# Performance work log

Hardware: AMD Instinct MI355X
Metric: run time of the kernel (lower is better)

The kernel has to match this reference:

```python
import jax, jax.numpy as jnp
import numpy as np
from jax import lax

INPUT_SIZE = 16384
NUM_CONV = 128
KMAX = 11  # max kernel size from {7, 9, 11}
BATCH = 256


def setup_inputs() -> dict:
    # Mirror FeatureExtractor._generate_random_params / _generate_random_convolutions
    rng = np.random.RandomState(0)
    kernel_sizes = rng.choice([7, 9, 11], NUM_CONV)
    dilations, paddings = [], []
    W = np.zeros((NUM_CONV, KMAX), np.float32)  # zero-padded kernel bank
    b = np.zeros((NUM_CONV,), np.float32)
    for i, k in enumerate(kernel_sizes):
        d_f = 2.0 ** rng.uniform(0.0, np.log2((INPUT_SIZE - 1) / (k - 1)))
        p = (k - 1) * d_f // 2 if rng.randint(2) else 0
        dilations.append(int(d_f))
        paddings.append(int(p))
        w = rng.normal(0.0, 1.0, k)
        w = w - w.mean()  # centered kernel ('normal' sampling type)
        W[i, :k] = w.astype(np.float32)
        b[i] = rng.uniform(-1.0, 1.0)
    key = jax.random.key(0)
    x = jax.random.normal(key, (BATCH, 1, INPUT_SIZE), dtype=jnp.float32)
    return {
        "x": x,
        "weights": jnp.asarray(W),
        "biases": jnp.asarray(b),
        "kernel_sizes": np.asarray(kernel_sizes, np.int64),
        "dilations": np.asarray(dilations, np.int64),
        "paddings": np.asarray(paddings, np.int64),
    }


def reference(x, weights, biases, kernel_sizes, dilations, paddings):
    # x: [B, 1, L]. Each conv has its own (k, dilation, padding) -> distinct
    # output lengths, so a Python loop over the fixed NUM_CONV structurally
    # distinct convs is required (matches the original module).
    feats = []
    n = weights.shape[0]
    for i in range(n):
        k = int(kernel_sizes[i])
        d = int(dilations[i])
        p = int(paddings[i])
        w = weights[i, :k].reshape(1, 1, k)  # OIW
        # torch Conv1d = cross-correlation with rhs (kernel) dilation
        y = lax.conv_general_dilated(
            x, w, window_strides=(1,), padding=[(p, p)], rhs_dilation=(d,)
        ) + biases[i]
        fm = y[:, 0, :]                      # [B, L_out]
        mx = fm.max(axis=-1)                 # global max pool
        ppv = (fm >= 0).sum(axis=-1) / fm.shape[-1]  # proportion of positives
        feats.append(jnp.stack([mx, ppv.astype(x.dtype)], axis=-1))  # [B, 2]
    out = jnp.concatenate(feats, axis=-1)    # [B, 2*num_conv], interleaved (max, ppv)
    return out.reshape(out.shape[0], 1, out.shape[1])  # [B, 1, 2*num_conv]
```

## Files before the change

### kernel.cpp

```cpp
#include <hip/hip_runtime.h>
#include <math.h>

#define S_LEN   16384
#define NCONV   128
#define NBATCH  256
#define TPB     1024
#define NGRP    8
#define ZSLOT   16384
#define DSTRIDE 24
#define BIGQ    (1 << 28)

typedef float __attribute__((address_space(1))) as1_float;
typedef float __attribute__((address_space(3))) as3_float;
typedef __attribute__((ext_vector_type(2))) float f2;
typedef unsigned long long u64;

__global__ void setup_desc(const int* __restrict__ ks, const int* __restrict__ dil,
                           const int* __restrict__ pad, const float* __restrict__ W,
                           const float* __restrict__ bias, int* __restrict__ ws)
{
  __shared__ int cost_s[NCONV];
  __shared__ int grp_s[NCONV];
  const int ci = threadIdx.x;
  const int is64 = (ks[1] == 0);
  const int k = is64 ? ks[2 * ci]  : ks[ci];
  const int d = is64 ? dil[2 * ci] : dil[ci];
  const int p = is64 ? pad[2 * ci] : pad[ci];
  const int L = S_LEN + 2 * p - d * (k - 1);
  const int A = L / d, B = L - A * d;
  int cost = L * (k + 9) + d * k * 3;
  if (d == 1) cost += L * (k + 9);
  cost_s[ci] = cost;
  __syncthreads();
  int rank = 0;
  for (int j = 0; j < NCONV; ++j) {
    const int cj = cost_s[j];
    rank += (cj > cost) || (cj == cost && j < ci);
  }
  int gg = rank & 7;
  if ((rank >> 3) & 1) gg = 7 - gg;
  grp_s[ci] = gg;
  __syncthreads();
  int rho = 0;
  for (int j = 0; j < NCONV; ++j) {
    if (grp_s[j] != gg) continue;
    const int cj = cost_s[j];
    rho += (cj > cost) || (cj == cost && j < ci);
  }
#pragma unroll
  for (int h = 0; h < 2; ++h) {
    const int j2 = 2 * rho + h;
    const int wv = (j2 < 16) ? j2 : 31 - j2;
    const int sq = (j2 < 16) ? 0 : 1;
    int* dsc = ws + (gg * 32 + wv * 2 + sq) * DSTRIDE;
    dsc[0] = d; dsc[1] = p; dsc[2] = A; dsc[3] = B;
    dsc[4] = ci; dsc[5] = rho; dsc[6] = h; dsc[7] = k;
    ((float*)dsc)[8] = 1.0f / (float)L;
    ((float*)dsc)[9] = bias[ci];
#pragma unroll
    for (int t = 0; t < 11; ++t) ((float*)dsc)[10 + t] = W[ci * 11 + t];
  }
}

__device__ __forceinline__ float sgpr_f(float v) {
  return __int_as_float(__builtin_amdgcn_readfirstlane(__float_as_int(v)));
}
__device__ __forceinline__ int sgpr_i(int v) {
  return __builtin_amdgcn_readfirstlane(v);
}
__device__ __forceinline__ float rcpf(float x) { return __builtin_amdgcn_rcpf(x); }

__device__ __forceinline__ int divq(int num, float rd, int d) {
  int q = (int)((float)num * rd);
  q -= (q * d > num);
  q += ((q + 1) * d <= num);
  return q;
}

__device__ __forceinline__ float lds_at(const float* sh, int pos) {
  unsigned idx = (unsigned)pos;
  idx = idx > (unsigned)ZSLOT ? (unsigned)ZSLOT : idx;
  return sh[idx];
}
__device__ __forceinline__ f2 rd2(const float* sh, int pos) {
  unsigned idx = (unsigned)pos;
  idx = idx > (unsigned)ZSLOT ? (unsigned)ZSLOT : idx;
  f2 v; v.x = sh[idx]; v.y = sh[idx + 1];
  return v;
}

__device__ __forceinline__ f2 pfma(f2 a, f2 b, f2 c) {
#if __has_builtin(__builtin_elementwise_fma)
  return __builtin_elementwise_fma(a, b, c);
#else
  f2 r; r.x = fmaf(a.x, b.x, c.x); r.y = fmaf(a.y, b.y, c.y); return r;
#endif
}
__device__ __forceinline__ f2 pmax(f2 a, f2 b) {
#if __has_builtin(__builtin_elementwise_max)
  return __builtin_elementwise_max(a, b);
#else
  f2 r; r.x = fmaxf(a.x, b.x); r.y = fmaxf(a.y, b.y); return r;
#endif
}

template <int K>
__device__ __forceinline__ void pwalk(
    const float* sh, const u64* wu, float bval,
    int d, int sb, int q0, int q1, f2& mxv, int& ca, int& cb)
{
  const int n = q1 - q0;
  if (n <= 0) return;
  f2 win[K];
  int pos = sb + q0 * d;
#pragma unroll
  for (int t = 0; t < K - 1; ++t) { win[t] = rd2(sh, pos); pos += d; }
  f2 bb; bb.x = bval; bb.y = bval;
  int i = 0;
  for (; i + K <= n; i += K) {
#pragma unroll
    for (int s = 0; s < K; ++s) {
      const f2 cur = rd2(sh, pos); pos += d;
      f2 a = bb;
#pragma unroll
      for (int t = 0; t < K; ++t) {
        const f2 wv = __builtin_bit_cast(f2, wu[t]);
        a = pfma(wv, (t == K - 1) ? cur : win[(s + t) % K], a);
      }
      win[(s + K - 1) % K] = cur;
      mxv = pmax(mxv, a);
      ca += (a.x >= 0.f); cb += (a.y >= 0.f);
    }
  }
  const int rem = n - i;
  if (rem > 0) {
#pragma unroll
    for (int s = 0; s < K - 1; ++s) {
      const f2 cur = rd2(sh, pos); pos += d;
      f2 a = bb;
#pragma unroll
      for (int t = 0; t < K; ++t) {
        const f2 wv = __builtin_bit_cast(f2, wu[t]);
        a = pfma(wv, (t == K - 1) ? cur : win[(s + t) % K], a);
      }
      win[(s + K - 1) % K] = cur;
      if (s < rem) { mxv = pmax(mxv, a); ca += (a.x >= 0.f); cb += (a.y >= 0.f); }
    }
  }
}

__device__ __forceinline__ void swalk(
    const float* sh, const float* w, float bval,
    int d, int sb, int q0, int q1, float& mx, int& cnt)
{
  const int n = q1 - q0;
  if (n <= 0) return;
  float win[11];
  int pos = sb + q0 * d;
#pragma unroll
  for (int t = 0; t < 10; ++t) { win[t] = lds_at(sh, pos); pos += d; }
  int i = 0;
  for (; i + 11 <= n; i += 11) {
#pragma unroll
    for (int s = 0; s < 11; ++s) {
      win[(s + 10) % 11] = lds_at(sh, pos); pos += d;
      float a = bval;
#pragma unroll
      for (int t = 0; t < 11; ++t) a = fmaf(w[t], win[(s + t) % 11], a);
      mx = fmaxf(mx, a); cnt += (a >= 0.f);
    }
  }
  const int rem = n - i;
  if (rem > 0) {
#pragma unroll
    for (int s = 0; s < 10; ++s) {
      win[(s + 10) % 11] = lds_at(sh, pos); pos += d;
      float a = bval;
#pragma unroll
      for (int t = 0; t < 11; ++t) a = fmaf(w[t], win[(s + t) % 11], a);
      if (s < rem) { mx = fmaxf(mx, a); cnt += (a >= 0.f); }
    }
  }
}

__device__ __forceinline__ void scalar_split(
    const float* sh, const float* w, float bval,
    int d, int p, int r, int c0, int c1, int lane, float& mx, int& cnt)
{
  const int n = c1 - c0;
  if (n <= 0) return;
  const int v  = lane;
  const int mm = n >> 6;
  const int sA = (mm >= 32) ? (v & 31) : (((v & 31) * mm) >> 5);
  const int vB = v + 1;
  const int sB = (mm >= 32) ? (vB & 31) : (((vB & 31) * mm) >> 5);
  const int q0 = c0 + (int)(((long long)n * v) >> 6) + sA;
  const int q1 = (v == 63) ? c1 : c0 + (int)(((long long)n * vB) >> 6) + sB;
  swalk(sh, w, bval, d, r - p, q0, q1, mx, cnt);
}

template <int K>
__device__ __forceinline__ void one_out(
    const float* sh, const float* w, float bval,
    int d, int p, int j, float& mx, int& cnt)
{
  float a = bval;
  int pos = j - p;
#pragma unroll
  for (int t = 0; t < K; ++t) { a = fmaf(w[t], lds_at(sh, pos), a); pos += d; }
  mx = fmaxf(mx, a); cnt += (a >= 0.f);
}

template <int K>
__device__ __forceinline__ void conv_chunk(
    const float* sh, const u64* wu, const float* w, float bval,
    int d, int p, int A, int B, int h, int lane,
    f2& mxv, float& mxs, int& ca, int& cb)
{
  if (d == 1) {
    const int H = (A + 1) >> 1;
    scalar_split(sh, w, bval, 1, p, 0, h ? H : 0, h ? A : H, lane, mxs, ca);
    return;
  }
  const int npair = d >> 1;
  if (npair >= 128) {
    const int half = npair >> 1;
    const int g0 = h ? half : 0;
    const int g1 = h ? npair : half;
    for (int c = g0 + lane; c < g1; c += 64) {
      const int r0 = 2 * c;
      const int Qm = A + (r0 + 1 < B);
      pwalk<K>(sh, wu, bval, d, r0 - p, 0, Qm, mxv, ca, cb);
      if (B == r0 + 1) one_out<K>(sh, w, bval, d, p, r0 + A * d, mxs, ca);
    }
  } else if (npair >= 64) {
    const int H = (A + 1) >> 1;
    const int c0 = h ? H : 0;
    const int c1 = h ? BIGQ : H;
    for (int c = lane; c < npair; c += 64) {
      const int r0 = 2 * c;
      const int Qm = A + (r0 + 1 < B);
      pwalk<K>(sh, wu, bval, d, r0 - p, c0, min(c1, Qm), mxv, ca, cb);
      if (B == r0 + 1 && A >= c0 && A < c1)
        one_out<K>(sh, w, bval, d, p, r0 + A * d, mxs, ca);
    }
  } else {
    const int H = (A + 1) >> 1;
    const int c0 = h ? H : 0;
    const int c1h = h ? BIGQ : H;
    const float rdp = rcpf((float)npair);
    int v  = (int)((float)lane * rdp);
    int g2 = lane - v * npair;
    if (g2 < 0)           { --v; g2 += npair; }
    else if (g2 >= npair) { ++v; g2 -= npair; }
    const int nv = divq(63 - g2, rdp, npair) + 1;
    const int r0 = 2 * g2;
    const int Qm = A + (r0 + 1 < B);
    const int cc1 = min(c1h, Qm);
    const int n = cc1 - c0;
    if (n > 0) {
      const float rn = rcpf((float)nv);
      const int mm = (int)((float)n * rn);
      const int sA = (mm >= 32) ? (v & 31) : (((v & 31) * mm) >> 5);
      const int vB = v + 1;
      const int sB = (mm >= 32) ? (vB & 31) : (((vB & 31) * mm) >> 5);
      const int q0 = c0 + (int)((float)(n * v) * rn) + sA;
      const int q1 = (v == nv - 1) ? cc1
                   : c0 + (int)((float)(n * vB) * rn) + sB;
      pwalk<K>(sh, wu, bval, d, r0 - p, q0, q1, mxv, ca, cb);
    }
    if (v == nv - 1 && B == r0 + 1 && A >= c0 && A < c1h)
      one_out<K>(sh, w, bval, d, p, r0 + A * d, mxs, ca);
  }
  if ((d & 1) && d > 1) {
    const int H2 = (A + 1) >> 1;
    const int r = d - 1;
    const int Qr = A + (r < B);
    const int c0 = h ? H2 : 0;
    const int c1 = h ? Qr : min(H2, Qr);
    scalar_split(sh, w, bval, d, p, r, c0, c1, lane, mxs, ca);
  }
}

__global__ __launch_bounds__(TPB, 8) void rocket_feats(
    const float* __restrict__ x, const int* __restrict__ ws,
    float* __restrict__ out)
{
  __shared__ float sh[S_LEN + 2];
  __shared__ float smx[2][16];
  __shared__ int   scn[2][16];
  __shared__ int   sci[16];
  __shared__ float sin_[16];

  const int tid  = threadIdx.x;
  const int blk  = blockIdx.x;
  const int g    = blk & 7;
  const int b    = blk >> 3;
  const int lane = tid & 63, wid = tid >> 6;

  const float* xrow = x + (size_t)b * S_LEN;
  {
    const float* gb = xrow + lane * 4;
#pragma unroll
    for (int c = 0; c < 4; ++c) {
      const int off = (wid * 4 + c) * 256;
      __builtin_amdgcn_global_load_lds((const as1_float*)(gb + off),
                                       (as3_float*)(sh + off), 16, 0, 0);
    }
  }
  if (tid == 0) { sh[ZSLOT] = 0.f; sh[ZSLOT + 1] = 0.f; }
  __syncthreads();

  for (int sq = 0; sq < 2; ++sq) {
    const int* dsc = ws + (g * 32 + wid * 2 + sq) * DSTRIDE;
    const int d  = sgpr_i(dsc[0]);
    const int p  = sgpr_i(dsc[1]);
    const int A  = sgpr_i(dsc[2]);
    const int B  = sgpr_i(dsc[3]);
    const int ci = sgpr_i(dsc[4]);
    const int t_ = sgpr_i(dsc[5]);
    const int h  = sgpr_i(dsc[6]);
    const int k  = sgpr_i(dsc[7]);
    const float invL = sgpr_f(((const float*)dsc)[8]);
    const float bval = sgpr_f(((const float*)dsc)[9]);
    float wf[11]; u64 wu[11];
#pragma unroll
    for (int t = 0; t < 11; ++t) {
      wf[t] = sgpr_f(((const float*)dsc)[10 + t]);
      const unsigned wb = (unsigned)__float_as_int(wf[t]);
      wu[t] = ((u64)wb << 32) | (u64)wb;
    }

    f2 mxv; mxv.x = -INFINITY; mxv.y = -INFINITY;
    float mxs = -INFINITY;
    int ca = 0, cb = 0;

    if (k == 7)
      conv_chunk<7 >(sh, wu, wf, bval, d, p, A, B, h, lane, mxv, mxs, ca, cb);
    else if (k == 9)
      conv_chunk<9 >(sh, wu, wf, bval, d, p, A, B, h, lane, mxv, mxs, ca, cb);
    else
      conv_chunk<11>(sh, wu, wf, bval, d, p, A, B, h, lane, mxv, mxs, ca, cb);

    float mx = fmaxf(fmaxf(mxv.x, mxv.y), mxs);
    int cnt = ca + cb;
#pragma unroll
    for (int off = 32; off > 0; off >>= 1) {
      mx = fmaxf(mx, __shfl_down(mx, off, 64));
      cnt += __shfl_down(cnt, off, 64);
    }
    if (lane == 0) {
      smx[h][t_] = mx; scn[h][t_] = cnt;
      sci[t_] = ci; sin_[t_] = invL;
    }
  }

  __syncthreads();
  if (tid < 16) {
    const float m = fmaxf(smx[0][tid], smx[1][tid]);
    const int   c = scn[0][tid] + scn[1][tid];
    out[(size_t)b * (2 * NCONV) + 2 * sci[tid]]     = m;
    out[(size_t)b * (2 * NCONV) + 2 * sci[tid] + 1] = (float)c * sin_[tid];
  }
}

extern "C" void kernel_launch(void* const* d_in, const int* in_sizes, int n_in,
                              void* d_out, int out_size, void* d_ws, size_t ws_size,
                              hipStream_t stream) {
  const float* x    = (const float*)d_in[0];
  const float* W    = (const float*)d_in[1];
  const float* bias = (const float*)d_in[2];
  const int*   ks   = (const int*)d_in[3];
  const int*   dil  = (const int*)d_in[4];
  const int*   pad  = (const int*)d_in[5];
  float* out = (float*)d_out;
  int*   ws  = (int*)d_ws;

  hipLaunchKernelGGL(setup_desc, dim3(1), dim3(NCONV), 0, stream,
                     ks, dil, pad, W, bias, ws);
  hipLaunchKernelGGL(rocket_feats, dim3(NBATCH * NGRP), dim3(TPB), 0, stream,
                     x, ws, out);
}
```

Baseline: 297.6 us.

## Use wave-ballot counting, byte-offset LDS addressing, templated scalar walk and retuned cost model

Positive counts are now accumulated as wave-uniform scalar values using ballot plus popcount. This removes the per-lane integer adds and the shuffle reduction for counts, at the cost of a ballot per output. LDS addressing switches to precomputed byte offsets with a shifted buffer that has zero guard slots on both sides. This is meant to cut address arithmetic. The scalar walk is templated on kernel size so k=7/9 no longer do 11 taps, and the load-balancing cost model used for grouping convolutions is retuned.

```diff
diff --git a/kernel.cpp b/kernel.cpp
--- a/kernel.cpp
+++ b/kernel.cpp
@@ -6,9 +6,9 @@
 #define NBATCH  256
 #define TPB     1024
 #define NGRP    8
-#define ZSLOT   16384
 #define DSTRIDE 24
 #define BIGQ    (1 << 28)
+#define CLMP    65552u
 
 typedef float __attribute__((address_space(1))) as1_float;
 typedef float __attribute__((address_space(3))) as3_float;
@@ -28,8 +28,8 @@
   const int p = is64 ? pad[2 * ci] : pad[ci];
   const int L = S_LEN + 2 * p - d * (k - 1);
   const int A = L / d, B = L - A * d;
-  int cost = L * (k + 9) + d * k * 3;
-  if (d == 1) cost += L * (k + 9);
+  int cost = L * (k + 5) + ((d >= 128) ? (d >> 1) : 64) * (k - 1) * 2;
+  if (d == 1) cost = L * (k + 5) * 2;
   cost_s[ci] = cost;
   __syncthreads();
   int rank = 0;
@@ -77,16 +77,17 @@
   return q;
 }
 
-__device__ __forceinline__ float lds_at(const float* sh, int pos) {
-  unsigned idx = (unsigned)pos;
-  idx = idx > (unsigned)ZSLOT ? (unsigned)ZSLOT : idx;
-  return sh[idx];
-}
-__device__ __forceinline__ f2 rd2(const float* sh, int pos) {
-  unsigned idx = (unsigned)pos;
-  idx = idx > (unsigned)ZSLOT ? (unsigned)ZSLOT : idx;
-  f2 v; v.x = sh[idx]; v.y = sh[idx + 1];
+__device__ __forceinline__ f2 rd2b(const float* sh, int ib) {
+  unsigned u = (unsigned)ib;
+  u = u > CLMP ? CLMP : u;
+  const float* p = (const float*)((const char*)sh + u);
+  f2 v; v.x = p[0]; v.y = p[1];
   return v;
+}
+__device__ __forceinline__ float ld1b(const float* sh, int ib) {
+  unsigned u = (unsigned)ib;
+  u = u > CLMP ? CLMP : u;
+  return *(const float*)((const char*)sh + u);
 }
 
 __device__ __forceinline__ f2 pfma(f2 a, f2 b, f2 c) {
@@ -103,89 +104,108 @@
   f2 r; r.x = fmaxf(a.x, b.x); r.y = fmaxf(a.y, b.y); return r;
 #endif
 }
+__device__ __forceinline__ int wcount(bool pred) {
+  return (int)__popcll(__ballot(pred));
+}
 
 template <int K>
 __device__ __forceinline__ void pwalk(
-    const float* sh, const u64* wu, float bval,
-    int d, int sb, int q0, int q1, f2& mxv, int& ca, int& cb)
+    const float* sh, const u64* wu, const f2 bbv,
+    int d, int sb4, int q0, int q1, f2& mxv, int& cw)
 {
   const int n = q1 - q0;
   if (n <= 0) return;
   f2 win[K];
-  int pos = sb + q0 * d;
-#pragma unroll
-  for (int t = 0; t < K - 1; ++t) { win[t] = rd2(sh, pos); pos += d; }
-  f2 bb; bb.x = bval; bb.y = bval;
+  int bb = (sb4 + q0 * d) * 4;
+#pragma unroll
+  for (int t = 0; t < K - 1; ++t)
+    win[t] = rd2b(sh, bb + t * (d * 4));
+  bb += (K - 1) * (d * 4);
   int i = 0;
   for (; i + K <= n; i += K) {
 #pragma unroll
     for (int s = 0; s < K; ++s) {
-      const f2 cur = rd2(sh, pos); pos += d;
-      f2 a = bb;
-#pragma unroll
-      for (int t = 0; t < K; ++t) {
-        const f2 wv = __builtin_bit_cast(f2, wu[t]);
-        a = pfma(wv, (t == K - 1) ? cur : win[(s + t) % K], a);
-      }
+      const f2 cur = rd2b(sh, bb + s * (d * 4));
+      f2 a = pfma(__builtin_bit_cast(f2, wu[0]), win[s % K], bbv);
+#pragma unroll
+      for (int t = 1; t < K; ++t)
+        a = pfma(__builtin_bit_cast(f2, wu[t]),
+                 (t == K - 1) ? cur : win[(s + t) % K], a);
       win[(s + K - 1) % K] = cur;
       mxv = pmax(mxv, a);
-      ca += (a.x >= 0.f); cb += (a.y >= 0.f);
-    }
+      cw += wcount(a.x >= 0.f);
+      cw += wcount(a.y >= 0.f);
+    }
+    bb += K * (d * 4);
   }
   const int rem = n - i;
   if (rem > 0) {
 #pragma unroll
     for (int s = 0; s < K - 1; ++s) {
-      const f2 cur = rd2(sh, pos); pos += d;
-      f2 a = bb;
-#pragma unroll
-      for (int t = 0; t < K; ++t) {
-        const f2 wv = __builtin_bit_cast(f2, wu[t]);
-        a = pfma(wv, (t == K - 1) ? cur : win[(s + t) % K], a);
-      }
+      const f2 cur = rd2b(sh, bb + s * (d * 4));
+      f2 a = pfma(__builtin_bit_cast(f2, wu[0]), win[s % K], bbv);
+#pragma unroll
+      for (int t = 1; t < K; ++t)
+        a = pfma(__builtin_bit_cast(f2, wu[t]),
+                 (t == K - 1) ? cur : win[(s + t) % K], a);
       win[(s + K - 1) % K] = cur;
-      if (s < rem) { mxv = pmax(mxv, a); ca += (a.x >= 0.f); cb += (a.y >= 0.f); }
-    }
-  }
-}
-
+      const bool ok = (s < rem);
+      if (ok) mxv = pmax(mxv, a);
+      cw += wcount(ok && (a.x >= 0.f));
+      cw += wcount(ok && (a.y >= 0.f));
+    }
+  }
+}
+
+template <int K>
 __device__ __forceinline__ void swalk(
     const float* sh, const float* w, float bval,
-    int d, int sb, int q0, int q1, float& mx, int& cnt)
+    int d, int sb4, int q0, int q1, float& mx, int& cw)
 {
   const int n = q1 - q0;
   if (n <= 0) return;
-  float win[11];
-  int pos = sb + q0 * d;
-#pragma unroll
-  for (int t = 0; t < 10; ++t) { win[t] = lds_at(sh, pos); pos += d; }
+  float win[K];
+  int bb = (sb4 + q0 * d) * 4;
+#pragma unroll
+  for (int t = 0; t < K - 1; ++t)
+    win[t] = ld1b(sh, bb + t * (d * 4));
+  bb += (K - 1) * (d * 4);
   int i = 0;
-  for (; i + 11 <= n; i += 11) {
-#pragma unroll
-    for (int s = 0; s < 11; ++s) {
-      win[(s + 10) % 11] = lds_at(sh, pos); pos += d;
-      float a = bval;
-#pragma unroll
-      for (int t = 0; t < 11; ++t) a = fmaf(w[t], win[(s + t) % 11], a);
-      mx = fmaxf(mx, a); cnt += (a >= 0.f);
-    }
+  for (; i + K <= n; i += K) {
+#pragma unroll
+    for (int s = 0; s < K; ++s) {
+      const float cur = ld1b(sh, bb + s * (d * 4));
+      float a = fmaf(w[0], win[s % K], bval);
+#pragma unroll
+      for (int t = 1; t < K; ++t)
+        a = fmaf(w[t], (t == K - 1) ? cur : win[(s + t) % K], a);
+      win[(s + K - 1) % K] = cur;
+      mx = fmaxf(mx, a);
+      cw += wcount(a >= 0.f);
+    }
+    bb += K * (d * 4);
   }
   const int rem = n - i;
   if (rem > 0) {
 #pragma unroll
-    for (int s = 0; s < 10; ++s) {
-      win[(s + 10) % 11] = lds_at(sh, pos); pos += d;
-      float a = bval;
-#pragma unroll
-      for (int t = 0; t < 11; ++t) a = fmaf(w[t], win[(s + t) % 11], a);
-      if (s < rem) { mx = fmaxf(mx, a); cnt += (a >= 0.f); }
-    }
-  }
-}
-
+    for (int s = 0; s < K - 1; ++s) {
+      const float cur = ld1b(sh, bb + s * (d * 4));
+      float a = fmaf(w[0], win[s % K], bval);
+#pragma unroll
+      for (int t = 1; t < K; ++t)
+        a = fmaf(w[t], (t == K - 1) ? cur : win[(s + t) % K], a);
+      win[(s + K - 1) % K] = cur;
+      const bool ok = (s < rem);
+      if (ok) mx = fmaxf(mx, a);
+      cw += wcount(ok && (a >= 0.f));
+    }
+  }
+}
+
+template <int K>
 __device__ __forceinline__ void scalar_split(
     const float* sh, const float* w, float bval,
-    int d, int p, int r, int c0, int c1, int lane, float& mx, int& cnt)
+    int d, int p, int r, int c0, int c1, int lane, float& mx, int& cw)
 {
   const int n = c1 - c0;
   if (n <= 0) return;
@@ -196,30 +216,31 @@
   const int sB = (mm >= 32) ? (vB & 31) : (((vB & 31) * mm) >> 5);
   const int q0 = c0 + (int)(((long long)n * v) >> 6) + sA;
   const int q1 = (v == 63) ? c1 : c0 + (int)(((long long)n * vB) >> 6) + sB;
-  swalk(sh, w, bval, d, r - p, q0, q1, mx, cnt);
+  swalk<K>(sh, w, bval, d, r - p + 4, q0, q1, mx, cw);
 }
 
 template <int K>
 __device__ __forceinline__ void one_out(
     const float* sh, const float* w, float bval,
-    int d, int p, int j, float& mx, int& cnt)
+    int d, int p, int j, float& mx, int& cw)
 {
   float a = bval;
-  int pos = j - p;
-#pragma unroll
-  for (int t = 0; t < K; ++t) { a = fmaf(w[t], lds_at(sh, pos), a); pos += d; }
-  mx = fmaxf(mx, a); cnt += (a >= 0.f);
+  int bb = (j - p + 4) * 4;
+#pragma unroll
+  for (int t = 0; t < K; ++t) { a = fmaf(w[t], ld1b(sh, bb), a); bb += d * 4; }
+  mx = fmaxf(mx, a);
+  cw += wcount(a >= 0.f);
 }
 
 template <int K>
 __device__ __forceinline__ void conv_chunk(
-    const float* sh, const u64* wu, const float* w, float bval,
+    const float* sh, const u64* wu, const float* w, float bval, const f2 bbv,
     int d, int p, int A, int B, int h, int lane,
-    f2& mxv, float& mxs, int& ca, int& cb)
+    f2& mxv, float& mxs, int& cw)
 {
   if (d == 1) {
     const int H = (A + 1) >> 1;
-    scalar_split(sh, w, bval, 1, p, 0, h ? H : 0, h ? A : H, lane, mxs, ca);
+    scalar_split<K>(sh, w, bval, 1, p, 0, h ? H : 0, h ? A : H, lane, mxs, cw);
     return;
   }
   const int npair = d >> 1;
@@ -230,8 +251,8 @@
     for (int c = g0 + lane; c < g1; c += 64) {
       const int r0 = 2 * c;
       const int Qm = A + (r0 + 1 < B);
-      pwalk<K>(sh, wu, bval, d, r0 - p, 0, Qm, mxv, ca, cb);
-      if (B == r0 + 1) one_out<K>(sh, w, bval, d, p, r0 + A * d, mxs, ca);
+      pwalk<K>(sh, wu, bbv, d, r0 - p + 4, 0, Qm, mxv, cw);
+      if (B == r0 + 1) one_out<K>(sh, w, bval, d, p, r0 + A * d, mxs, cw);
     }
   } else if (npair >= 64) {
     const int H = (A + 1) >> 1;
@@ -240,9 +261,9 @@
     for (int c = lane; c < npair; c += 64) {
       const int r0 = 2 * c;
       const int Qm = A + (r0 + 1 < B);
-      pwalk<K>(sh, wu, bval, d, r0 - p, c0, min(c1, Qm), mxv, ca, cb);
+      pwalk<K>(sh, wu, bbv, d, r0 - p + 4, c0, min(c1, Qm), mxv, cw);
       if (B == r0 + 1 && A >= c0 && A < c1)
-        one_out<K>(sh, w, bval, d, p, r0 + A * d, mxs, ca);
+        one_out<K>(sh, w, bval, d, p, r0 + A * d, mxs, cw);
     }
   } else {
     const int H = (A + 1) >> 1;
@@ -267,10 +288,10 @@
       const int q0 = c0 + (int)((float)(n * v) * rn) + sA;
       const int q1 = (v == nv - 1) ? cc1
                    : c0 + (int)((float)(n * vB) * rn) + sB;
-      pwalk<K>(sh, wu, bval, d, r0 - p, q0, q1, mxv, ca, cb);
+      pwalk<K>(sh, wu, bbv, d, r0 - p + 4, q0, q1, mxv, cw);
     }
     if (v == nv - 1 && B == r0 + 1 && A >= c0 && A < c1h)
-      one_out<K>(sh, w, bval, d, p, r0 + A * d, mxs, ca);
+      one_out<K>(sh, w, bval, d, p, r0 + A * d, mxs, cw);
   }
   if ((d & 1) && d > 1) {
     const int H2 = (A + 1) >> 1;
@@ -278,7 +299,7 @@
     const int Qr = A + (r < B);
     const int c0 = h ? H2 : 0;
     const int c1 = h ? Qr : min(H2, Qr);
-    scalar_split(sh, w, bval, d, p, r, c0, c1, lane, mxs, ca);
+    scalar_split<K>(sh, w, bval, d, p, r, c0, c1, lane, mxs, cw);
   }
 }
 
@@ -286,7 +307,7 @@
     const float* __restrict__ x, const int* __restrict__ ws,
     float* __restrict__ out)
 {
-  __shared__ float sh[S_LEN + 2];
+  __shared__ float sh[S_LEN + 8];
   __shared__ float smx[2][16];
   __shared__ int   scn[2][16];
   __shared__ int   sci[16];
@@ -305,10 +326,11 @@
     for (int c = 0; c < 4; ++c) {
       const int off = (wid * 4 + c) * 256;
       __builtin_amdgcn_global_load_lds((const as1_float*)(gb + off),
-                                       (as3_float*)(sh + off), 16, 0, 0);
-    }
-  }
-  if (tid == 0) { sh[ZSLOT] = 0.f; sh[ZSLOT + 1] = 0.f; }
+                                       (as3_float*)(sh + 4 + off), 16, 0, 0);
+    }
+  }
+  if (tid < 4) sh[tid] = 0.f;
+  if (tid >= 4 && tid < 8) sh[S_LEN + tid] = 0.f;
   __syncthreads();
 
   for (int sq = 0; sq < 2; ++sq) {
@@ -330,27 +352,25 @@
       const unsigned wb = (unsigned)__float_as_int(wf[t]);
       wu[t] = ((u64)wb << 32) | (u64)wb;
     }
+    f2 bbv; bbv.x = bval; bbv.y = bval;
 
     f2 mxv; mxv.x = -INFINITY; mxv.y = -INFINITY;
     float mxs = -INFINITY;
-    int ca = 0, cb = 0;
+    int cw = 0;
 
     if (k == 7)
-      conv_chunk<7 >(sh, wu, wf, bval, d, p, A, B, h, lane, mxv, mxs, ca, cb);
+      conv_chunk<7 >(sh, wu, wf, bval, bbv, d, p, A, B, h, lane, mxv, mxs, cw);
     else if (k == 9)
-      conv_chunk<9 >(sh, wu, wf, bval, d, p, A, B, h, lane, mxv, mxs, ca, cb);
+      conv_chunk<9 >(sh, wu, wf, bval, bbv, d, p, A, B, h, lane, mxv, mxs, cw);
     else
-      conv_chunk<11>(sh, wu, wf, bval, d, p, A, B, h, lane, mxv, mxs, ca, cb);
+      conv_chunk<11>(sh, wu, wf, bval, bbv, d, p, A, B, h, lane, mxv, mxs, cw);
 
     float mx = fmaxf(fmaxf(mxv.x, mxv.y), mxs);
-    int cnt = ca + cb;
-#pragma unroll
-    for (int off = 32; off > 0; off >>= 1) {
+#pragma unroll
+    for (int off = 32; off > 0; off >>= 1)
       mx = fmaxf(mx, __shfl_down(mx, off, 64));
-      cnt += __shfl_down(cnt, off, 64);
-    }
     if (lane == 0) {
-      smx[h][t_] = mx; scn[h][t_] = cnt;
+      smx[h][t_] = mx; scn[h][t_] = cw;
       sci[t_] = ci; sin_[t_] = invL;
     }
   }
```

After: 270.8 us. 9.0% less time.
